# Kernel tuning notes

Hardware: AMD Instinct MI355X
Metric: run time of the kernel (lower is better)

## Reference

```python
import jax, jax.numpy as jnp
import numpy as np

EPS = 1e-5

def layernorm(x, gamma, beta):
    mu = jnp.mean(x, axis=-1, keepdims=True)
    var = jnp.mean(jnp.square(x - mu), axis=-1, keepdims=True)
    return (x - mu) * jax.lax.rsqrt(var + EPS) * gamma + beta

def setup_inputs() -> dict:
    key = jax.random.key(0)
    ks = jax.random.split(key, 5)
    B, I, H = 8192, 1024, 1024
    x = jax.random.normal(ks[0], (B, I), dtype=jnp.float32)
    hx = jax.random.normal(ks[1], (B, H), dtype=jnp.float32)
    cx = jax.random.normal(ks[2], (B, H), dtype=jnp.float32)
    W_ih = jax.random.normal(ks[3], (4 * H, I), dtype=jnp.float32)
    W_hh = jax.random.normal(ks[4], (4 * H, H), dtype=jnp.float32)
    gamma_i = jnp.ones((4 * H,), jnp.float32); beta_i = jnp.zeros((4 * H,), jnp.float32)
    gamma_h = jnp.ones((4 * H,), jnp.float32); beta_h = jnp.zeros((4 * H,), jnp.float32)
    gamma_c = jnp.ones((H,), jnp.float32); beta_c = jnp.zeros((H,), jnp.float32)
    return {"x": x, "hx": hx, "cx": cx, "W_ih": W_ih, "W_hh": W_hh,
            "gamma_i": gamma_i, "beta_i": beta_i,
            "gamma_h": gamma_h, "beta_h": beta_h,
            "gamma_c": gamma_c, "beta_c": beta_c}

def reference(x, hx, cx, W_ih, W_hh, gamma_i, beta_i, gamma_h, beta_h, gamma_c, beta_c):
    # igates/hgates: [B, 4H]
    igates = layernorm(x @ W_ih.T, gamma_i, beta_i)
    hgates = layernorm(hx @ W_hh.T, gamma_h, beta_h)
    gates = igates + hgates
    i, f, g, o = jnp.split(gates, 4, axis=1)
    i = jax.nn.sigmoid(i)
    f = jax.nn.sigmoid(f)
    g = jnp.tanh(g)
    o = jax.nn.sigmoid(o)
    cy = layernorm(f * cx + i * g, gamma_c, beta_c)
    hy = o * jnp.tanh(cy)
    return (hy, (hy, cy))
```

## Files before the change

### kernel.cpp

```cpp
#include <hip/hip_runtime.h>

typedef __attribute__((ext_vector_type(8))) short short8_t;
typedef __attribute__((ext_vector_type(4))) float f32x4;

#define AS1 __attribute__((address_space(1)))
#define AS3 __attribute__((address_space(3)))

__device__ inline void gload_lds16(const void* g, void* l) {
  __builtin_amdgcn_global_load_lds((AS1 void*)g, (AS3 void*)l, 16, 0, 0);
}

__device__ inline unsigned short f2bf(float f) {
  unsigned int u = __builtin_bit_cast(unsigned int, f);
  u += 0x7fffu + ((u >> 16) & 1u);
  return (unsigned short)(u >> 16);
}
__device__ inline float bfu2f(unsigned short u) {
  return __builtin_bit_cast(float, ((unsigned int)u) << 16);
}
__device__ inline float sigmoidf_(float x) {
  x = fminf(fmaxf(x, -30.f), 30.f);
  return 1.f / (1.f + __expf(-x));
}
__device__ inline float tanhf_(float x) {
  x = fminf(fmaxf(x, -15.f), 15.f);
  float e = __expf(2.f * x);
  return (e - 1.f) / (e + 1.f);
}

__global__ __launch_bounds__(256) void cvt_bf16_all(
    const float* __restrict__ x,  unsigned short* __restrict__ xb,
    const float* __restrict__ hx, unsigned short* __restrict__ hxb,
    const float* __restrict__ Wi, unsigned short* __restrict__ wib,
    const float* __restrict__ Wh, unsigned short* __restrict__ whb) {
  int blk = blockIdx.x;
  const float* src; unsigned short* dst;
  if (blk < 4096)       { src = x;  dst = xb; }
  else if (blk < 8192)  { src = hx; dst = hxb; blk -= 4096; }
  else if (blk < 10240) { src = Wi; dst = wib; blk -= 8192; }
  else                  { src = Wh; dst = whb; blk -= 10240; }
  int i = (blk * 256 + threadIdx.x) * 8;
  const float4* s = reinterpret_cast<const float4*>(src + i);
  float4 a = s[0], b = s[1];
  union { unsigned short us[8]; uint4 v; } o;
  o.us[0] = f2bf(a.x); o.us[1] = f2bf(a.y); o.us[2] = f2bf(a.z); o.us[3] = f2bf(a.w);
  o.us[4] = f2bf(b.x); o.us[5] = f2bf(b.y); o.us[6] = f2bf(b.z); o.us[7] = f2bf(b.w);
  *reinterpret_cast<uint4*>(dst + i) = o.v;
}

__global__ __launch_bounds__(512, 2) void gemm_dual(
    const unsigned short* __restrict__ Xb, const unsigned short* __restrict__ Hxb,
    const unsigned short* __restrict__ Wib, const unsigned short* __restrict__ Whb,
    unsigned short* __restrict__ Gi, unsigned short* __restrict__ Gh) {
  const int K = 1024, N = 4096, NT = 16;
  const unsigned short* A  = blockIdx.z ? Hxb : Xb;
  const unsigned short* Bw = blockIdx.z ? Whb : Wib;
  unsigned short* C        = blockIdx.z ? Gh : Gi;

  __shared__ __align__(16) unsigned short lA[2 * 2 * 128 * 64];
  __shared__ __align__(16) unsigned short lB[2 * 2 * 128 * 64];

  const int t    = threadIdx.x;
  const int wid  = t >> 6;
  const int lane = t & 63;
  const int fr = lane & 15, fq = lane >> 4;
  const int wm = wid >> 2;
  const int wn = wid & 3;
  const int m0 = blockIdx.y * 256, n0 = blockIdx.x * 256;

  auto stage = [&](int kt, int X, int h) {
    if (kt >= NT) return;
    const unsigned short* G = X ? Bw : A;
    const int r0 = (X ? n0 : m0) + h * 128;
    unsigned short* L = (X ? lB : lA) + (kt & 1) * 16384 + h * 8192;
#pragma unroll
    for (int g = 0; g < 2; ++g) {
      int idx = g * 512 + t;
      int row = idx >> 3;
      int ls  = (idx & 7) ^ (row & 7);
      gload_lds16(G + (size_t)(r0 + row) * K + kt * 64 + ls * 8,
                  L + g * 4096 + wid * 512);
    }
  };

  f32x4 acc[8][4];
#pragma unroll
  for (int i = 0; i < 8; ++i)
#pragma unroll
    for (int j = 0; j < 4; ++j) acc[i][j] = (f32x4){0.f, 0.f, 0.f, 0.f};

  stage(0, 0, 0); stage(0, 0, 1); stage(0, 1, 0); stage(0, 1, 1);
  stage(1, 0, 0); stage(1, 0, 1);
  asm volatile("s_waitcnt vmcnt(4)");
  __builtin_amdgcn_s_barrier();

  const int sw0 = ((fq)     ^ (fr & 7)) * 8;
  const int sw1 = ((fq + 4) ^ (fr & 7)) * 8;
  const int bro = (wn & 1) * 64;

  short8_t av[4][2], bv[4][2];

  for (int kt = 0; kt < NT; ++kt) {
    const unsigned short* As = lA + (kt & 1) * 16384 + wm * 8192;
    const unsigned short* Bs = lB + (kt & 1) * 16384 + (wn >> 1) * 8192;

#pragma unroll
    for (int m = 0; m < 4; ++m) {
      av[m][0] = *reinterpret_cast<const short8_t*>(As + (m * 16 + fr) * 64 + sw0);
      av[m][1] = *reinterpret_cast<const short8_t*>(As + (m * 16 + fr) * 64 + sw1);
    }
#pragma unroll
    for (int n = 0; n < 2; ++n) {
      bv[n][0] = *reinterpret_cast<const short8_t*>(Bs + (bro + n * 16 + fr) * 64 + sw0);
      bv[n][1] = *reinterpret_cast<const short8_t*>(Bs + (bro + n * 16 + fr) * 64 + sw1);
    }
    stage(kt + 1, 1, 0);
    asm volatile("s_waitcnt lgkmcnt(8)");
    __builtin_amdgcn_s_barrier();
    asm volatile("s_waitcnt lgkmcnt(0)");
    __builtin_amdgcn_s_setprio(1);
#pragma unroll
    for (int m = 0; m < 4; ++m)
#pragma unroll
      for (int n = 0; n < 2; ++n)
#pragma unroll
        for (int ks = 0; ks < 2; ++ks)
          acc[m][n] = __builtin_amdgcn_mfma_f32_16x16x32_bf16(av[m][ks], bv[n][ks], acc[m][n], 0, 0, 0);
    __builtin_amdgcn_s_setprio(0);
    __builtin_amdgcn_s_barrier();

#pragma unroll
    for (int n = 2; n < 4; ++n) {
      bv[n][0] = *reinterpret_cast<const short8_t*>(Bs + (bro + n * 16 + fr) * 64 + sw0);
      bv[n][1] = *reinterpret_cast<const short8_t*>(Bs + (bro + n * 16 + fr) * 64 + sw1);
    }
    stage(kt + 1, 1, 1);
    __builtin_amdgcn_s_barrier();
    asm volatile("s_waitcnt lgkmcnt(0)");
    __builtin_amdgcn_s_setprio(1);
#pragma unroll
    for (int m = 0; m < 4; ++m)
#pragma unroll
      for (int n = 2; n < 4; ++n)
#pragma unroll
        for (int ks = 0; ks < 2; ++ks)
          acc[m][n] = __builtin_amdgcn_mfma_f32_16x16x32_bf16(av[m][ks], bv[n][ks], acc[m][n], 0, 0, 0);
    __builtin_amdgcn_s_setprio(0);
    __builtin_amdgcn_s_barrier();

#pragma unroll
    for (int m = 0; m < 4; ++m) {
      av[m][0] = *reinterpret_cast<const short8_t*>(As + ((m + 4) * 16 + fr) * 64 + sw0);
      av[m][1] = *reinterpret_cast<const short8_t*>(As + ((m + 4) * 16 + fr) * 64 + sw1);
    }
    __builtin_amdgcn_s_barrier();
    asm volatile("s_waitcnt lgkmcnt(0)");
    __builtin_amdgcn_s_setprio(1);
#pragma unroll
    for (int m = 0; m < 4; ++m)
#pragma unroll
      for (int n = 0; n < 2; ++n)
#pragma unroll
        for (int ks = 0; ks < 2; ++ks)
          acc[m + 4][n] = __builtin_amdgcn_mfma_f32_16x16x32_bf16(av[m][ks], bv[n][ks], acc[m + 4][n], 0, 0, 0);
    __builtin_amdgcn_s_setprio(0);
    __builtin_amdgcn_s_barrier();

    stage(kt + 2, 0, 0);
    stage(kt + 2, 0, 1);
    __builtin_amdgcn_s_barrier();
    asm volatile("s_waitcnt lgkmcnt(0)");
    __builtin_amdgcn_s_setprio(1);
#pragma unroll
    for (int m = 0; m < 4; ++m)
#pragma unroll
      for (int n = 2; n < 4; ++n)
#pragma unroll
        for (int ks = 0; ks < 2; ++ks)
          acc[m + 4][n] = __builtin_amdgcn_mfma_f32_16x16x32_bf16(av[m][ks], bv[n][ks], acc[m + 4][n], 0, 0, 0);
    __builtin_amdgcn_s_setprio(0);
    if (kt + 2 < NT) {
      asm volatile("s_waitcnt vmcnt(4)");
    } else if (kt + 1 < NT) {
      asm volatile("s_waitcnt vmcnt(0)");
    }
    __builtin_amdgcn_s_barrier();
  }

#pragma unroll
  for (int m = 0; m < 8; ++m)
#pragma unroll
    for (int n = 0; n < 4; ++n)
#pragma unroll
      for (int r = 0; r < 4; ++r) {
        int row = m0 + wm * 128 + m * 16 + fq * 4 + r;
        int col = n0 + wn * 64 + n * 16 + fr;
        C[(size_t)row * N + col] = f2bf(acc[m][n][r]);
      }
}

__global__ __launch_bounds__(256) void fuse_ln_lstm(
    const unsigned short* __restrict__ Gi, const unsigned short* __restrict__ Gh,
    const float* __restrict__ cx,
    const float* __restrict__ gi_g, const float* __restrict__ gi_b,
    const float* __restrict__ gh_g, const float* __restrict__ gh_b,
    const float* __restrict__ gc_g, const float* __restrict__ gc_b,
    float* __restrict__ out) {
  const int H = 1024;
  const size_t BH = (size_t)8192 * 1024;
  const int b = blockIdx.x, t = threadIdx.x;
  const int wid = t >> 6, lane = t & 63;

  __shared__ __align__(16) unsigned short lgi[4096];
  __shared__ __align__(16) unsigned short lgh[4096];
  __shared__ float lred[32];

  const uint4* gi_row = reinterpret_cast<const uint4*>(Gi) + (size_t)b * 512;
  const uint4* gh_row = reinterpret_cast<const uint4*>(Gh) + (size_t)b * 512;

  float si = 0.f, qi = 0.f, sh = 0.f, qh = 0.f;
#pragma unroll
  for (int c = 0; c < 2; ++c) {
    uint4 v = gi_row[c * 256 + t];
    uint4 w = gh_row[c * 256 + t];
    *reinterpret_cast<uint4*>(&lgi[(c * 256 + t) * 8]) = v;
    *reinterpret_cast<uint4*>(&lgh[(c * 256 + t) * 8]) = w;
    unsigned int uv[4] = {v.x, v.y, v.z, v.w};
    unsigned int uw[4] = {w.x, w.y, w.z, w.w};
#pragma unroll
    for (int e = 0; e < 4; ++e) {
      float a0 = __builtin_bit_cast(float, uv[e] << 16);
      float a1 = __builtin_bit_cast(float, uv[e] & 0xffff0000u);
      si += a0 + a1; qi += a0 * a0 + a1 * a1;
      float b0 = __builtin_bit_cast(float, uw[e] << 16);
      float b1 = __builtin_bit_cast(float, uw[e] & 0xffff0000u);
      sh += b0 + b1; qh += b0 * b0 + b1 * b1;
    }
  }
#pragma unroll
  for (int s = 32; s; s >>= 1) {
    si += __shfl_xor(si, s); qi += __shfl_xor(qi, s);
    sh += __shfl_xor(sh, s); qh += __shfl_xor(qh, s);
  }
  if (lane == 0) { lred[wid] = si; lred[4 + wid] = qi; lred[8 + wid] = sh; lred[12 + wid] = qh; }
  __syncthreads();
  float Si = lred[0] + lred[1] + lred[2] + lred[3];
  float Qi = lred[4] + lred[5] + lred[6] + lred[7];
  float Sh = lred[8] + lred[9] + lred[10] + lred[11];
  float Qh = lred[12] + lred[13] + lred[14] + lred[15];
  const float inv4096 = 1.f / 4096.f;
  float mui = Si * inv4096;
  float rsi = rsqrtf(fmaxf(Qi * inv4096 - mui * mui, 0.f) + 1e-5f);
  float muh = Sh * inv4096;
  float rsh = rsqrtf(fmaxf(Qh * inv4096 - muh * muh, 0.f) + 1e-5f);

  float cv[4], ov[4];
  float sc = 0.f, qc = 0.f;
#pragma unroll
  for (int k = 0; k < 4; ++k) {
    int h = t + 256 * k;
    float g0 = bfu2f(lgi[h]),        h0 = bfu2f(lgh[h]);
    float g1 = bfu2f(lgi[h + 1024]), h1 = bfu2f(lgh[h + 1024]);
    float g2 = bfu2f(lgi[h + 2048]), h2 = bfu2f(lgh[h + 2048]);
    float g3 = bfu2f(lgi[h + 3072]), h3 = bfu2f(lgh[h + 3072]);
    float vi = (g0 - mui) * rsi * gi_g[h]        + gi_b[h]        + (h0 - muh) * rsh * gh_g[h]        + gh_b[h];
    float vf = (g1 - mui) * rsi * gi_g[h + 1024] + gi_b[h + 1024] + (h1 - muh) * rsh * gh_g[h + 1024] + gh_b[h + 1024];
    float vg = (g2 - mui) * rsi * gi_g[h + 2048] + gi_b[h + 2048] + (h2 - muh) * rsh * gh_g[h + 2048] + gh_b[h + 2048];
    float vo = (g3 - mui) * rsi * gi_g[h + 3072] + gi_b[h + 3072] + (h3 - muh) * rsh * gh_g[h + 3072] + gh_b[h + 3072];
    float ig = sigmoidf_(vi), fg = sigmoidf_(vf), gg = tanhf_(vg), og = sigmoidf_(vo);
    float c = fg * cx[(size_t)b * H + h] + ig * gg;
    cv[k] = c; ov[k] = og;
    sc += c; qc += c * c;
  }
#pragma unroll
  for (int s = 32; s; s >>= 1) { sc += __shfl_xor(sc, s); qc += __shfl_xor(qc, s); }
  if (lane == 0) { lred[16 + wid] = sc; lred[20 + wid] = qc; }
  __syncthreads();
  float Sc = lred[16] + lred[17] + lred[18] + lred[19];
  float Qc = lred[20] + lred[21] + lred[22] + lred[23];
  const float inv1024 = 1.f / 1024.f;
  float muc = Sc * inv1024;
  float rsc = rsqrtf(fmaxf(Qc * inv1024 - muc * muc, 0.f) + 1e-5f);
#pragma unroll
  for (int k = 0; k < 4; ++k) {
    int h = t + 256 * k;
    float cy = (cv[k] - muc) * rsc * gc_g[h] + gc_b[h];
    float hy = ov[k] * tanhf_(cy);
    size_t o0 = (size_t)b * H + h;
    out[o0] = hy;
    out[BH + o0] = hy;
    out[2 * BH + o0] = cy;
  }
}

extern "C" void kernel_launch(void* const* d_in, const int* in_sizes, int n_in,
                              void* d_out, int out_size, void* d_ws, size_t ws_size,
                              hipStream_t stream) {
  const float* x    = (const float*)d_in[0];
  const float* hx   = (const float*)d_in[1];
  const float* cx   = (const float*)d_in[2];
  const float* Wih  = (const float*)d_in[3];
  const float* Whh  = (const float*)d_in[4];
  const float* gi_g = (const float*)d_in[5];
  const float* gi_b = (const float*)d_in[6];
  const float* gh_g = (const float*)d_in[7];
  const float* gh_b = (const float*)d_in[8];
  const float* gc_g = (const float*)d_in[9];
  const float* gc_b = (const float*)d_in[10];
  float* out = (float*)d_out;

  const size_t NB = (size_t)8192 * 1024;
  const size_t NW = (size_t)4096 * 1024;
  const size_t NG = (size_t)8192 * 4096;

  unsigned short* ws  = (unsigned short*)d_ws;
  unsigned short* xb  = ws;
  unsigned short* hxb = xb + NB;
  unsigned short* wib = hxb + NB;
  unsigned short* whb = wib + NW;
  unsigned short* Gi  = whb + NW;
  unsigned short* Gh  = Gi + NG;

  cvt_bf16_all<<<12288, 256, 0, stream>>>(x, xb, hx, hxb, Wih, wib, Whh, whb);

  dim3 gg(4096 / 256, 8192 / 256, 2);
  gemm_dual<<<gg, 512, 0, stream>>>(xb, hxb, wib, whb, Gi, Gh);

  fuse_ln_lstm<<<8192, 256, 0, stream>>>(Gi, Gh, cx, gi_g, gi_b, gh_g, gh_b,
                                         gc_g, gc_b, out);
}
```

Before: 238.2 us.

## Switch GEMM to 32x32x16 MFMA tiles and remap blocks for L2 locality

Replaces the 16x16x32 bf16 MFMA sub-tiles with 32x32x16 instructions, so each wave holds 4x2 accumulators of 16 floats instead of 8x4 of 4. The LDS fragment loads, swizzle offsets, staging order and epilogue row/column mapping change to match. Block indices are also remapped so that consecutive workgroups are spread across groups of eight, changing which tiles run together and how they share L2 or per-XCD cache. The larger MFMA needs fewer instructions and fewer LDS reads per FLOP, but it changes register pressure and the interleaving of loads with compute.

```diff
diff --git a/kernel.cpp b/kernel.cpp
--- a/kernel.cpp
+++ b/kernel.cpp
@@ -1,7 +1,7 @@
 #include <hip/hip_runtime.h>
 
 typedef __attribute__((ext_vector_type(8))) short short8_t;
-typedef __attribute__((ext_vector_type(4))) float f32x4;
+typedef __attribute__((ext_vector_type(16))) float f32x16;
 
 #define AS1 __attribute__((address_space(1)))
 #define AS3 __attribute__((address_space(3)))
@@ -53,9 +53,14 @@
     const unsigned short* __restrict__ Wib, const unsigned short* __restrict__ Whb,
     unsigned short* __restrict__ Gi, unsigned short* __restrict__ Gh) {
   const int K = 1024, N = 4096, NT = 16;
-  const unsigned short* A  = blockIdx.z ? Hxb : Xb;
-  const unsigned short* Bw = blockIdx.z ? Whb : Wib;
-  unsigned short* C        = blockIdx.z ? Gh : Gi;
+
+  int lin = blockIdx.x + 16 * blockIdx.y + 512 * blockIdx.z;
+  int nid = (lin & 7) * 128 + (lin >> 3);
+  const int bz = nid >> 9, by = (nid >> 4) & 31, bx = nid & 15;
+
+  const unsigned short* A  = bz ? Hxb : Xb;
+  const unsigned short* Bw = bz ? Whb : Wib;
+  unsigned short* C        = bz ? Gh : Gi;
 
   __shared__ __align__(16) unsigned short lA[2 * 2 * 128 * 64];
   __shared__ __align__(16) unsigned short lB[2 * 2 * 128 * 64];
@@ -63,10 +68,11 @@
   const int t    = threadIdx.x;
   const int wid  = t >> 6;
   const int lane = t & 63;
-  const int fr = lane & 15, fq = lane >> 4;
+  const int r31  = lane & 31;
+  const int l5   = lane >> 5;
   const int wm = wid >> 2;
   const int wn = wid & 3;
-  const int m0 = blockIdx.y * 256, n0 = blockIdx.x * 256;
+  const int m0 = by * 256, n0 = bx * 256;
 
   auto stage = [&](int kt, int X, int h) {
     if (kt >= NT) return;
@@ -83,101 +89,92 @@
     }
   };
 
-  f32x4 acc[8][4];
-#pragma unroll
-  for (int i = 0; i < 8; ++i)
-#pragma unroll
-    for (int j = 0; j < 4; ++j) acc[i][j] = (f32x4){0.f, 0.f, 0.f, 0.f};
+  f32x16 acc[4][2];
+#pragma unroll
+  for (int i = 0; i < 4; ++i)
+#pragma unroll
+    for (int j = 0; j < 2; ++j)
+#pragma unroll
+      for (int r = 0; r < 16; ++r) acc[i][j][r] = 0.f;
 
   stage(0, 0, 0); stage(0, 0, 1); stage(0, 1, 0); stage(0, 1, 1);
   stage(1, 0, 0); stage(1, 0, 1);
   asm volatile("s_waitcnt vmcnt(4)");
   __builtin_amdgcn_s_barrier();
 
-  const int sw0 = ((fq)     ^ (fr & 7)) * 8;
-  const int sw1 = ((fq + 4) ^ (fr & 7)) * 8;
+  int sw[4];
+#pragma unroll
+  for (int ks = 0; ks < 4; ++ks) sw[ks] = ((ks * 2 + l5) ^ (lane & 7)) * 8;
   const int bro = (wn & 1) * 64;
 
-  short8_t av[4][2], bv[4][2];
+  short8_t a01[2][4], a23[2][4], bn[4];
 
   for (int kt = 0; kt < NT; ++kt) {
     const unsigned short* As = lA + (kt & 1) * 16384 + wm * 8192;
     const unsigned short* Bs = lB + (kt & 1) * 16384 + (wn >> 1) * 8192;
 
 #pragma unroll
-    for (int m = 0; m < 4; ++m) {
-      av[m][0] = *reinterpret_cast<const short8_t*>(As + (m * 16 + fr) * 64 + sw0);
-      av[m][1] = *reinterpret_cast<const short8_t*>(As + (m * 16 + fr) * 64 + sw1);
-    }
-#pragma unroll
-    for (int n = 0; n < 2; ++n) {
-      bv[n][0] = *reinterpret_cast<const short8_t*>(Bs + (bro + n * 16 + fr) * 64 + sw0);
-      bv[n][1] = *reinterpret_cast<const short8_t*>(Bs + (bro + n * 16 + fr) * 64 + sw1);
-    }
+    for (int mi = 0; mi < 2; ++mi)
+#pragma unroll
+      for (int ks = 0; ks < 4; ++ks)
+        a01[mi][ks] = *reinterpret_cast<const short8_t*>(As + (mi * 32 + r31) * 64 + sw[ks]);
+#pragma unroll
+    for (int ks = 0; ks < 4; ++ks)
+      bn[ks] = *reinterpret_cast<const short8_t*>(Bs + (bro + r31) * 64 + sw[ks]);
     stage(kt + 1, 1, 0);
     asm volatile("s_waitcnt lgkmcnt(8)");
     __builtin_amdgcn_s_barrier();
     asm volatile("s_waitcnt lgkmcnt(0)");
     __builtin_amdgcn_s_setprio(1);
 #pragma unroll
-    for (int m = 0; m < 4; ++m)
-#pragma unroll
-      for (int n = 0; n < 2; ++n)
-#pragma unroll
-        for (int ks = 0; ks < 2; ++ks)
-          acc[m][n] = __builtin_amdgcn_mfma_f32_16x16x32_bf16(av[m][ks], bv[n][ks], acc[m][n], 0, 0, 0);
+    for (int mi = 0; mi < 2; ++mi)
+#pragma unroll
+      for (int ks = 0; ks < 4; ++ks)
+        acc[mi][0] = __builtin_amdgcn_mfma_f32_32x32x16_bf16(a01[mi][ks], bn[ks], acc[mi][0], 0, 0, 0);
     __builtin_amdgcn_s_setprio(0);
     __builtin_amdgcn_s_barrier();
 
 #pragma unroll
-    for (int n = 2; n < 4; ++n) {
-      bv[n][0] = *reinterpret_cast<const short8_t*>(Bs + (bro + n * 16 + fr) * 64 + sw0);
-      bv[n][1] = *reinterpret_cast<const short8_t*>(Bs + (bro + n * 16 + fr) * 64 + sw1);
-    }
+    for (int mi = 0; mi < 2; ++mi)
+#pragma unroll
+      for (int ks = 0; ks < 4; ++ks)
+        a23[mi][ks] = *reinterpret_cast<const short8_t*>(As + ((mi + 2) * 32 + r31) * 64 + sw[ks]);
     stage(kt + 1, 1, 1);
     __builtin_amdgcn_s_barrier();
     asm volatile("s_waitcnt lgkmcnt(0)");
     __builtin_amdgcn_s_setprio(1);
 #pragma unroll
-    for (int m = 0; m < 4; ++m)
-#pragma unroll
-      for (int n = 2; n < 4; ++n)
-#pragma unroll
-        for (int ks = 0; ks < 2; ++ks)
-          acc[m][n] = __builtin_amdgcn_mfma_f32_16x16x32_bf16(av[m][ks], bv[n][ks], acc[m][n], 0, 0, 0);
+    for (int mi = 0; mi < 2; ++mi)
+#pragma unroll
+      for (int ks = 0; ks < 4; ++ks)
+        acc[mi + 2][0] = __builtin_amdgcn_mfma_f32_32x32x16_bf16(a23[mi][ks], bn[ks], acc[mi + 2][0], 0, 0, 0);
     __builtin_amdgcn_s_setprio(0);
     __builtin_amdgcn_s_barrier();
 
 #pragma unroll
-    for (int m = 0; m < 4; ++m) {
-      av[m][0] = *reinterpret_cast<const short8_t*>(As + ((m + 4) * 16 + fr) * 64 + sw0);
-      av[m][1] = *reinterpret_cast<const short8_t*>(As + ((m + 4) * 16 + fr) * 64 + sw1);
-    }
+    for (int ks = 0; ks < 4; ++ks)
+      bn[ks] = *reinterpret_cast<const short8_t*>(Bs + (bro + 32 + r31) * 64 + sw[ks]);
+    stage(kt + 2, 0, 0);
     __builtin_amdgcn_s_barrier();
     asm volatile("s_waitcnt lgkmcnt(0)");
     __builtin_amdgcn_s_setprio(1);
 #pragma unroll
-    for (int m = 0; m < 4; ++m)
-#pragma unroll
-      for (int n = 0; n < 2; ++n)
-#pragma unroll
-        for (int ks = 0; ks < 2; ++ks)
-          acc[m + 4][n] = __builtin_amdgcn_mfma_f32_16x16x32_bf16(av[m][ks], bv[n][ks], acc[m + 4][n], 0, 0, 0);
+    for (int mi = 0; mi < 2; ++mi)
+#pragma unroll
+      for (int ks = 0; ks < 4; ++ks)
+        acc[mi][1] = __builtin_amdgcn_mfma_f32_32x32x16_bf16(a01[mi][ks], bn[ks], acc[mi][1], 0, 0, 0);
     __builtin_amdgcn_s_setprio(0);
     __builtin_amdgcn_s_barrier();
 
-    stage(kt + 2, 0, 0);
     stage(kt + 2, 0, 1);
     __builtin_amdgcn_s_barrier();
     asm volatile("s_waitcnt lgkmcnt(0)");
     __builtin_amdgcn_s_setprio(1);
 #pragma unroll
-    for (int m = 0; m < 4; ++m)
-#pragma unroll
-      for (int n = 2; n < 4; ++n)
-#pragma unroll
-        for (int ks = 0; ks < 2; ++ks)
-          acc[m + 4][n] = __builtin_amdgcn_mfma_f32_16x16x32_bf16(av[m][ks], bv[n][ks], acc[m + 4][n], 0, 0, 0);
+    for (int mi = 0; mi < 2; ++mi)
+#pragma unroll
+      for (int ks = 0; ks < 4; ++ks)
+        acc[mi + 2][1] = __builtin_amdgcn_mfma_f32_32x32x16_bf16(a23[mi][ks], bn[ks], acc[mi + 2][1], 0, 0, 0);
     __builtin_amdgcn_s_setprio(0);
     if (kt + 2 < NT) {
       asm volatile("s_waitcnt vmcnt(4)");
@@ -188,14 +185,14 @@
   }
 
 #pragma unroll
-  for (int m = 0; m < 8; ++m)
-#pragma unroll
-    for (int n = 0; n < 4; ++n)
-#pragma unroll
-      for (int r = 0; r < 4; ++r) {
-        int row = m0 + wm * 128 + m * 16 + fq * 4 + r;
-        int col = n0 + wn * 64 + n * 16 + fr;
-        C[(size_t)row * N + col] = f2bf(acc[m][n][r]);
+  for (int mi = 0; mi < 4; ++mi)
+#pragma unroll
+    for (int nj = 0; nj < 2; ++nj)
+#pragma unroll
+      for (int r = 0; r < 16; ++r) {
+        int row = m0 + wm * 128 + mi * 32 + (r & 3) + 8 * (r >> 2) + 4 * l5;
+        int col = n0 + wn * 64 + nj * 32 + r31;
+        C[(size_t)row * N + col] = f2bf(acc[mi][nj][r]);
       }
 }
 
```

Result: slower. 255.1 us (+7.1%).
